# Kernel tuning notes

Measured on AMD Instinct MI355X. Metric: run time of the kernel, lower is better.

The kernel has to match this reference:

```python
import jax, jax.numpy as jnp
import numpy as np
import math

D_MODEL = 1024
NUM_HEADS = 16
NUM_LAYERS = 4
D_FF = 4096
TEXT_DIM = 512
B, SV, ST = 4, 2048, 100
EPS = 1e-5


def positional_encoding(seq_len, d):
    pos = jnp.arange(seq_len, dtype=jnp.float32)[:, None]
    div = jnp.exp(jnp.arange(0, d, 2, dtype=jnp.float32) * (-math.log(10000.0) / d))
    pe = jnp.zeros((seq_len, d), dtype=jnp.float32)
    pe = pe.at[:, 0::2].set(jnp.sin(pos * div))
    pe = pe.at[:, 1::2].set(jnp.cos(pos * div))
    return pe  # [seq_len, d]


def layer_norm(x, g, b):
    mu = jnp.mean(x, axis=-1, keepdims=True)
    var = jnp.mean(jnp.square(x - mu), axis=-1, keepdims=True)
    return (x - mu) * jax.lax.rsqrt(var + EPS) * g + b


def setup_inputs() -> dict:
    key = jax.random.key(0)
    ks = jax.random.split(key, 24)
    s = 0.02
    inp = {
        "video": jax.random.normal(ks[0], (B, SV, D_MODEL), jnp.float32),
        "text": jax.random.normal(ks[1], (B, ST, TEXT_DIM), jnp.float32),
        "text_mask": jnp.ones((B, ST), jnp.int32),
        # stacked per-layer params, weights stored [in, out]
        "Wq_w": jax.random.normal(ks[2], (NUM_LAYERS, D_MODEL, D_MODEL)) * s,
        "Wq_b": jnp.zeros((NUM_LAYERS, D_MODEL)),
        "Wk_w": jax.random.normal(ks[3], (NUM_LAYERS, TEXT_DIM, D_MODEL)) * s,
        "Wk_b": jnp.zeros((NUM_LAYERS, D_MODEL)),
        "Wv_w": jax.random.normal(ks[4], (NUM_LAYERS, TEXT_DIM, D_MODEL)) * s,
        "Wv_b": jnp.zeros((NUM_LAYERS, D_MODEL)),
        "Wo_w": jax.random.normal(ks[5], (NUM_LAYERS, D_MODEL, D_MODEL)) * s,
        "Wo_b": jnp.zeros((NUM_LAYERS, D_MODEL)),
        "fc1_w": jax.random.normal(ks[6], (NUM_LAYERS, D_MODEL, D_FF)) * s,
        "fc1_b": jnp.zeros((NUM_LAYERS, D_FF)),
        "fc2_w": jax.random.normal(ks[7], (NUM_LAYERS, D_FF, D_MODEL)) * s,
        "fc2_b": jnp.zeros((NUM_LAYERS, D_MODEL)),
        "n2_g": jnp.ones((NUM_LAYERS, D_MODEL)),
        "n2_b": jnp.zeros((NUM_LAYERS, D_MODEL)),
        "n3_g": jnp.ones((NUM_LAYERS, D_MODEL)),
        "n3_b": jnp.zeros((NUM_LAYERS, D_MODEL)),
    }
    return inp


def cross_attn_layer(video, text, mask, wq, bq, wk, bk, wv, bv, wo, bo):
    Bv, Sq, D = video.shape
    H, dk = NUM_HEADS, D_MODEL // NUM_HEADS
    q = (video @ wq + bq).reshape(Bv, Sq, H, dk).transpose(0, 2, 1, 3)  # bhqd
    k = (text @ wk + bk).reshape(Bv, -1, H, dk).transpose(0, 2, 1, 3)   # bhkd
    v = (text @ wv + bv).reshape(Bv, -1, H, dk).transpose(0, 2, 1, 3)
    scores = jnp.einsum("bhqd,bhkd->bhqk", q, k) / math.sqrt(dk)
    scores = jnp.where(mask, scores, jnp.float32(-1e9))
    probs = jax.nn.softmax(scores, axis=-1)
    out = jnp.einsum("bhqk,bhkd->bhqd", probs, v)
    out = out.transpose(0, 2, 1, 3).reshape(Bv, Sq, D)
    return out @ wo + bo


def reference(video, text, text_mask, Wq_w, Wq_b, Wk_w, Wk_b, Wv_w, Wv_b,
              Wo_w, Wo_b, fc1_w, fc1_b, fc2_w, fc2_b, n2_g, n2_b, n3_g, n3_b):
    video = video + positional_encoding(SV, D_MODEL)[None, :video.shape[1]]
    text = text + positional_encoding(ST, TEXT_DIM)[None, :text.shape[1]]
    mask = (text_mask != 0)[:, None, None, :]  # [B,1,1,St]
    for l in range(NUM_LAYERS):
        attn = cross_attn_layer(video, text, mask,
                                Wq_w[l], Wq_b[l], Wk_w[l], Wk_b[l],
                                Wv_w[l], Wv_b[l], Wo_w[l], Wo_b[l])
        video = layer_norm(video + attn, n2_g[l], n2_b[l])
        ff = jax.nn.relu(video @ fc1_w[l] + fc1_b[l]) @ fc2_w[l] + fc2_b[l]
        video = layer_norm(video + ff, n3_g[l], n3_b[l])
    return video
```

## Files before the change

### kernel.cpp

```cpp
#include <hip/hip_runtime.h>
#include <cstdint>
#include <cstddef>

typedef unsigned short u16;
typedef __attribute__((ext_vector_type(8))) __bf16 bf16x8;
typedef __attribute__((ext_vector_type(4))) float f32x4;

__device__ __forceinline__ f32x4 mfma_16x16x32(bf16x8 a, bf16x8 b, f32x4 c) {
  return __builtin_amdgcn_mfma_f32_16x16x32_bf16(a, b, c, 0, 0, 0);
}

__device__ __forceinline__ u16 f2bf(float f) {
  union { float f; uint32_t u; } c; c.f = f;
  uint32_t u = c.u + 0x7FFFu + ((c.u >> 16) & 1u);
  return (u16)(u >> 16);
}

__device__ __forceinline__ float bf2f(u16 x) {
  union { uint32_t u; float f; } c; c.u = ((uint32_t)x) << 16;
  return c.f;
}

__device__ __forceinline__ void gload_lds16(const void* g, void* l) {
  __builtin_amdgcn_global_load_lds(
      (__attribute__((address_space(1))) void*)(uintptr_t)g,
      (__attribute__((address_space(3))) void*)l, 16, 0, 0);
}

template<bool OUT_BF16, bool RELU, bool ACC>
__global__ __launch_bounds__(512, 2) void gemm8p(
    const u16* __restrict__ A, int lda, const u16* __restrict__ Bt, int ldb,
    const float* __restrict__ bias, void* Cout, int ldc,
    int M, int N, int K)
{
  constexpr int BM = 256, BN = 128, BK = 64;
  constexpr int TILE = (BM + BN) * BK;
  __shared__ u16 lds[3 * TILE];

  const int tid = threadIdx.x;
  const int lane = tid & 63, wave = tid >> 6;
  const int wm = wave >> 1, wn = wave & 1;
  const int m0 = blockIdx.x * BM, n0 = blockIdx.y * BN;

  const u16* gA[4];
  const u16* gB[2];
  #pragma unroll
  for (int i = 0; i < 4; i++) {
    int c = tid + i * 512, r = c >> 3, q = c & 7;
    gA[i] = A + (size_t)(m0 + r) * lda + ((q ^ (r & 7)) * 8);
  }
  #pragma unroll
  for (int i = 0; i < 2; i++) {
    int c = tid + i * 512, r = c >> 3, q = c & 7;
    gB[i] = Bt + (size_t)(n0 + r) * ldb + ((q ^ (r & 7)) * 8);
  }

  const int NT = K >> 6;

  auto STAGE = [&](int t, int buf, int piece) {
    u16* Sb = &lds[buf * TILE];
    const int ko = t * 64;
    if (piece == 0) {
      gload_lds16(gA[0] + ko, Sb + tid * 8);
      gload_lds16(gA[1] + ko, Sb + (tid + 512) * 8);
    } else if (piece == 1) {
      gload_lds16(gA[2] + ko, Sb + (tid + 1024) * 8);
      gload_lds16(gA[3] + ko, Sb + (tid + 1536) * 8);
    } else {
      gload_lds16(gB[0] + ko, Sb + BM * 64 + tid * 8);
      gload_lds16(gB[1] + ko, Sb + BM * 64 + (tid + 512) * 8);
    }
  };

  const int fr = lane & 15, g = lane >> 4;
  const int sx = fr & 7;

  f32x4 acc[4][4];
  #pragma unroll
  for (int m = 0; m < 4; m++)
    #pragma unroll
    for (int n = 0; n < 4; n++) acc[m][n] = f32x4{0.f, 0.f, 0.f, 0.f};

  STAGE(0, 0, 0); STAGE(0, 0, 1); STAGE(0, 0, 2);
  STAGE(1, 1, 0); STAGE(1, 1, 1); STAGE(1, 1, 2);
  asm volatile("s_waitcnt vmcnt(6)" ::: "memory");
  __builtin_amdgcn_s_barrier();
  __builtin_amdgcn_sched_barrier(0);

  int cur = 0;
  for (int t = 0; t < NT; ++t) {
    const u16* As = &lds[cur * TILE];
    const u16* Bs = As + BM * 64;
    const bool st = (t + 2 < NT);
    int sbuf = cur + 2; if (sbuf >= 3) sbuf -= 3;

    bf16x8 bf[4], afA[2], afB[2];
    const int arow0 = wm * 64 + fr;
    const int brow0 = wn * 64 + fr;

    #pragma unroll
    for (int nf = 0; nf < 4; nf++)
      bf[nf] = *(const bf16x8*)(Bs + (brow0 + nf * 16) * 64 + ((g ^ sx) * 8));
    #pragma unroll
    for (int mf = 0; mf < 2; mf++)
      afA[mf] = *(const bf16x8*)(As + (arow0 + mf * 16) * 64 + ((g ^ sx) * 8));
    if (st) STAGE(t + 2, sbuf, 0);
    __builtin_amdgcn_s_barrier();
    asm volatile("s_waitcnt lgkmcnt(0)" ::: "memory");
    __builtin_amdgcn_sched_barrier(0);
    __builtin_amdgcn_s_setprio(1);
    #pragma unroll
    for (int mf = 0; mf < 2; mf++)
      #pragma unroll
      for (int nf = 0; nf < 4; nf++)
        acc[mf][nf] = mfma_16x16x32(afA[mf], bf[nf], acc[mf][nf]);
    __builtin_amdgcn_s_setprio(0);
    __builtin_amdgcn_s_barrier();

    #pragma unroll
    for (int mf = 0; mf < 2; mf++)
      afB[mf] = *(const bf16x8*)(As + (arow0 + (mf + 2) * 16) * 64 + ((g ^ sx) * 8));
    if (st) STAGE(t + 2, sbuf, 1);
    __builtin_amdgcn_s_barrier();
    asm volatile("s_waitcnt lgkmcnt(0)" ::: "memory");
    __builtin_amdgcn_sched_barrier(0);
    __builtin_amdgcn_s_setprio(1);
    #pragma unroll
    for (int mf = 0; mf < 2; mf++)
      #pragma unroll
      for (int nf = 0; nf < 4; nf++)
        acc[mf + 2][nf] = mfma_16x16x32(afB[mf], bf[nf], acc[mf + 2][nf]);
    __builtin_amdgcn_s_setprio(0);
    __builtin_amdgcn_s_barrier();

    #pragma unroll
    for (int nf = 0; nf < 4; nf++)
      bf[nf] = *(const bf16x8*)(Bs + (brow0 + nf * 16) * 64 + (((4 + g) ^ sx) * 8));
    #pragma unroll
    for (int mf = 0; mf < 2; mf++)
      afA[mf] = *(const bf16x8*)(As + (arow0 + mf * 16) * 64 + (((4 + g) ^ sx) * 8));
    if (st) STAGE(t + 2, sbuf, 2);
    __builtin_amdgcn_s_barrier();
    asm volatile("s_waitcnt lgkmcnt(0)" ::: "memory");
    __builtin_amdgcn_sched_barrier(0);
    __builtin_amdgcn_s_setprio(1);
    #pragma unroll
    for (int mf = 0; mf < 2; mf++)
      #pragma unroll
      for (int nf = 0; nf < 4; nf++)
        acc[mf][nf] = mfma_16x16x32(afA[mf], bf[nf], acc[mf][nf]);
    __builtin_amdgcn_s_setprio(0);
    __builtin_amdgcn_s_barrier();

    #pragma unroll
    for (int mf = 0; mf < 2; mf++)
      afB[mf] = *(const bf16x8*)(As + (arow0 + (mf + 2) * 16) * 64 + (((4 + g) ^ sx) * 8));
    __builtin_amdgcn_s_barrier();
    asm volatile("s_waitcnt lgkmcnt(0)" ::: "memory");
    __builtin_amdgcn_sched_barrier(0);
    __builtin_amdgcn_s_setprio(1);
    #pragma unroll
    for (int mf = 0; mf < 2; mf++)
      #pragma unroll
      for (int nf = 0; nf < 4; nf++)
        acc[mf + 2][nf] = mfma_16x16x32(afB[mf], bf[nf], acc[mf + 2][nf]);
    __builtin_amdgcn_s_setprio(0);
    if (st) asm volatile("s_waitcnt vmcnt(6)" ::: "memory");
    else    asm volatile("s_waitcnt vmcnt(0)" ::: "memory");
    __builtin_amdgcn_sched_barrier(0);
    __builtin_amdgcn_s_barrier();
    __builtin_amdgcn_sched_barrier(0);

    cur = cur + 1 == 3 ? 0 : cur + 1;
  }

  #pragma unroll
  for (int nf = 0; nf < 4; nf++) {
    const int gcol = n0 + wn * 64 + nf * 16 + fr;
    const float bv = bias ? bias[gcol] : 0.f;
    #pragma unroll
    for (int mf = 0; mf < 4; mf++) {
      #pragma unroll
      for (int r = 0; r < 4; r++) {
        const int grow = m0 + wm * 64 + mf * 16 + g * 4 + r;
        float v = acc[mf][nf][r] + bv;
        if (ACC) v += bf2f(((const u16*)Cout)[(size_t)grow * ldc + gcol]);
        if (RELU) v = fmaxf(v, 0.f);
        if (OUT_BF16) ((u16*)Cout)[(size_t)grow * ldc + gcol] = f2bf(v);
        else         ((float*)Cout)[(size_t)grow * ldc + gcol] = v;
      }
    }
  }
}

template<bool TRANS>
__global__ __launch_bounds__(256, 2) void gemm_bt(
    const u16* __restrict__ A, int lda, const u16* __restrict__ Bt, int ldb,
    const float* __restrict__ bias, u16* Cout, int ldc,
    int M, int N, int K)
{
  __shared__ u16 ldsA[128 * 32];
  __shared__ u16 ldsB[128 * 32];

  const int tid = threadIdx.x;
  const int lane = tid & 63, wave = tid >> 6;
  const int wr = wave >> 1, wc = wave & 1;
  const int m0 = blockIdx.x * 128, n0 = blockIdx.y * 128;

  const int c0 = tid, c1 = tid + 256;
  const int ar0 = c0 >> 2, ak0 = (c0 & 3) * 8;
  const int ar1 = c1 >> 2, ak1 = (c1 & 3) * 8;

  const bool av0 = (m0 + ar0) < M;
  const bool av1 = (m0 + ar1) < M;
  const u16* Ag0 = A + (size_t)(m0 + ar0) * lda + ak0;
  const u16* Ag1 = A + (size_t)(m0 + ar1) * lda + ak1;
  const u16* Bg0 = Bt + (size_t)(n0 + ar0) * ldb + ak0;
  const u16* Bg1 = Bt + (size_t)(n0 + ar1) * ldb + ak1;

  f32x4 acc[4][4] = {};
  const int fr = lane & 15, fo = (lane >> 4) * 8;

  for (int k0 = 0; k0 < K; k0 += 32) {
    if (av0) gload_lds16(Ag0 + k0, &ldsA[c0 * 8]);
    if (av1) gload_lds16(Ag1 + k0, &ldsA[c1 * 8]);
    gload_lds16(Bg0 + k0, &ldsB[c0 * 8]);
    gload_lds16(Bg1 + k0, &ldsB[c1 * 8]);
    asm volatile("s_waitcnt vmcnt(0)" ::: "memory");
    __syncthreads();

    bf16x8 af[4], bfr[4];
    #pragma unroll
    for (int m = 0; m < 4; m++)
      af[m] = *(const bf16x8*)&ldsA[(wr * 64 + m * 16 + fr) * 32 + fo];
    #pragma unroll
    for (int n = 0; n < 4; n++)
      bfr[n] = *(const bf16x8*)&ldsB[(wc * 64 + n * 16 + fr) * 32 + fo];
    #pragma unroll
    for (int m = 0; m < 4; m++)
      #pragma unroll
      for (int n = 0; n < 4; n++)
        acc[m][n] = mfma_16x16x32(af[m], bfr[n], acc[m][n]);
    __syncthreads();
  }

  const int g = lane >> 4;
  #pragma unroll
  for (int m = 0; m < 4; m++) {
    #pragma unroll
    for (int n = 0; n < 4; n++) {
      const int gcol = n0 + wc * 64 + n * 16 + fr;
      const float bv = bias[gcol];
      #pragma unroll
      for (int r = 0; r < 4; r++) {
        const int grow = m0 + wr * 64 + m * 16 + g * 4 + r;
        if (grow < M) {
          float v = acc[m][n][r] + bv;
          if (TRANS) {
            int bb = grow / 100, jj = grow - bb * 100;
            int h = gcol >> 6, d = gcol & 63;
            Cout[(size_t)(((bb * 16 + h) * 64 + d)) * 128 + jj] = f2bf(v);
          } else {
            Cout[(size_t)grow * ldc + gcol] = f2bf(v);
          }
        }
      }
    }
  }
}

__global__ void wconv_t(const float* __restrict__ src, u16* __restrict__ dst,
                        int K, int N)
{
  __shared__ float tile[32][33];
  const int n0 = blockIdx.x * 32, k0 = blockIdx.y * 32;
  const int tx = threadIdx.x, ty = threadIdx.y;
  #pragma unroll
  for (int i = 0; i < 4; i++)
    tile[ty + i * 8][tx] = src[(size_t)(k0 + ty + i * 8) * N + n0 + tx];
  __syncthreads();
  #pragma unroll
  for (int i = 0; i < 4; i++)
    dst[(size_t)(n0 + ty + i * 8) * K + k0 + tx] = f2bf(tile[tx][ty + i * 8]);
}

__global__ __launch_bounds__(256) void pe_video_k(const float* __restrict__ video,
                                                  u16* __restrict__ vbf)
{
  const int r = blockIdx.x;
  const int s = r & 2047;
  const int d0 = threadIdx.x * 4;
  const size_t base = (size_t)r * 1024 + d0;
  float4 v = *(const float4*)&video[base];
  const float coef = -9.210340371976184f / 1024.f;
  float o[4];
  float in[4] = {v.x, v.y, v.z, v.w};
  #pragma unroll
  for (int i = 0; i < 4; i++) {
    int d = d0 + i;
    int j = d >> 1;
    float dv = expf((float)(2 * j) * coef);
    float arg = (float)s * dv;
    float pe = (d & 1) ? cosf(arg) : sinf(arg);
    o[i] = in[i] + pe;
  }
  uint2 pk;
  pk.x = (uint32_t)f2bf(o[0]) | ((uint32_t)f2bf(o[1]) << 16);
  pk.y = (uint32_t)f2bf(o[2]) | ((uint32_t)f2bf(o[3]) << 16);
  *(uint2*)&vbf[base] = pk;
}

__global__ __launch_bounds__(128) void pe_text_k(const float* __restrict__ text,
                                                 u16* __restrict__ tbf)
{
  const int r = blockIdx.x;
  const int s = r % 100;
  const int d0 = threadIdx.x * 4;
  const size_t base = (size_t)r * 512 + d0;
  float4 v = *(const float4*)&text[base];
  const float coef = -9.210340371976184f / 512.f;
  float o[4];
  float in[4] = {v.x, v.y, v.z, v.w};
  #pragma unroll
  for (int i = 0; i < 4; i++) {
    int d = d0 + i;
    int j = d >> 1;
    float dv = expf((float)(2 * j) * coef);
    float arg = (float)s * dv;
    float pe = (d & 1) ? cosf(arg) : sinf(arg);
    o[i] = in[i] + pe;
  }
  uint2 pk;
  pk.x = (uint32_t)f2bf(o[0]) | ((uint32_t)f2bf(o[1]) << 16);
  pk.y = (uint32_t)f2bf(o[2]) | ((uint32_t)f2bf(o[3]) << 16);
  *(uint2*)&tbf[base] = pk;
}

template<bool LAST>
__global__ __launch_bounds__(256) void ln2(const u16* __restrict__ xin,
                                           const u16* __restrict__ delta,
                                           const float* __restrict__ gamma,
                                           const float* __restrict__ beta,
                                           u16* __restrict__ xbf,
                                           float* __restrict__ fout)
{
  const int row = blockIdx.x;
  const size_t base = (size_t)row * 1024;
  const int t = threadIdx.x;
  const int d0 = t * 4;
  uint2 xv = *(const uint2*)&xin[base + d0];
  uint2 dv = *(const uint2*)&delta[base + d0];
  float v0 = bf2f((u16)(xv.x & 0xFFFF)) + bf2f((u16)(dv.x & 0xFFFF));
  float v1 = bf2f((u16)(xv.x >> 16))    + bf2f((u16)(dv.x >> 16));
  float v2 = bf2f((u16)(xv.y & 0xFFFF)) + bf2f((u16)(dv.y & 0xFFFF));
  float v3 = bf2f((u16)(xv.y >> 16))    + bf2f((u16)(dv.y >> 16));
  float s = v0 + v1 + v2 + v3;
  float q = v0 * v0 + v1 * v1 + v2 * v2 + v3 * v3;
  #pragma unroll
  for (int d = 32; d >= 1; d >>= 1) { s += __shfl_xor(s, d); q += __shfl_xor(q, d); }
  __shared__ float red[8];
  const int lane = t & 63, w = t >> 6;
  if (lane == 0) { red[w] = s; red[4 + w] = q; }
  __syncthreads();
  float S = red[0] + red[1] + red[2] + red[3];
  float Qs = red[4] + red[5] + red[6] + red[7];
  const float mu = S * (1.f / 1024.f);
  const float var = Qs * (1.f / 1024.f) - mu * mu;
  const float rs = rsqrtf(var + 1e-5f);
  float4 gv = *(const float4*)&gamma[d0];
  float4 bv = *(const float4*)&beta[d0];
  float o0 = (v0 - mu) * rs * gv.x + bv.x;
  float o1 = (v1 - mu) * rs * gv.y + bv.y;
  float o2 = (v2 - mu) * rs * gv.z + bv.z;
  float o3 = (v3 - mu) * rs * gv.w + bv.w;
  if (LAST) {
    *(float4*)&fout[base + d0] = make_float4(o0, o1, o2, o3);
  } else {
    uint2 pk;
    pk.x = (uint32_t)f2bf(o0) | ((uint32_t)f2bf(o1) << 16);
    pk.y = (uint32_t)f2bf(o2) | ((uint32_t)f2bf(o3) << 16);
    *(uint2*)&xbf[base + d0] = pk;
  }
}

__global__ __launch_bounds__(256) void attn_v2(
    const u16* __restrict__ Q, const u16* __restrict__ Kb,
    const u16* __restrict__ Vtb, const int* __restrict__ mask,
    u16* __restrict__ Out)
{
  __shared__ u16 ldsP[64 * 136];

  const int tid = threadIdx.x, lane = tid & 63, w = tid >> 6;
  const int qb = blockIdx.x, bh = blockIdx.y;
  const int b = bh >> 4, h = bh & 15;
  const int fr = lane & 15, g = lane >> 4, fo = g * 8;

  const size_t qrow = (size_t)(b * 2048 + qb * 64 + w * 16 + fr) * 1024 + h * 64;
  bf16x8 qf0 = *(const bf16x8*)&Q[qrow + fo];
  bf16x8 qf1 = *(const bf16x8*)&Q[qrow + 32 + fo];

  float madd[7];
  #pragma unroll
  for (int t = 0; t < 7; t++) {
    int col = t * 16 + fr;
    int mv = (col < 100) ? mask[b * 100 + col] : 0;
    madd[t] = mv ? 0.f : -1e30f;
  }

  float sc[7][4];
  #pragma unroll
  for (int t = 0; t < 7; t++) {
    int col = t * 16 + fr;
    int jr = (col < 100) ? col : 99;
    const u16* kp = Kb + (size_t)(b * 100 + jr) * 1024 + h * 64;
    bf16x8 kf0 = *(const bf16x8*)&kp[fo];
    bf16x8 kf1 = *(const bf16x8*)&kp[32 + fo];
    f32x4 a = {};
    a = mfma_16x16x32(qf0, kf0, a);
    a = mfma_16x16x32(qf1, kf1, a);
    #pragma unroll
    for (int r = 0; r < 4; r++)
      sc[t][r] = a[r] * 0.125f + madd[t];
  }

  #pragma unroll
  for (int r = 0; r < 4; r++) {
    float m = sc[0][r];
    #pragma unroll
    for (int t = 1; t < 7; t++) m = fmaxf(m, sc[t][r]);
    #pragma unroll
    for (int d = 8; d >= 1; d >>= 1) m = fmaxf(m, __shfl_xor(m, d));
    float ssum = 0.f;
    #pragma unroll
    for (int t = 0; t < 7; t++) { float p = __expf(sc[t][r] - m); sc[t][r] = p; ssum += p; }
    #pragma unroll
    for (int d = 8; d >= 1; d >>= 1) ssum += __shfl_xor(ssum, d);
    float is = 1.f / ssum;
    #pragma unroll
    for (int t = 0; t < 7; t++)
      ldsP[(w * 16 + g * 4 + r) * 136 + t * 16 + fr] = f2bf(sc[t][r] * is);
  }
  {
    u16* zp = &ldsP[(w * 16 + fr) * 136 + 112 + g * 6];
    #pragma unroll
    for (int i = 0; i < 6; i++) zp[i] = 0;
  }

  bf16x8 pa[4];
  #pragma unroll
  for (int kk = 0; kk < 4; kk++)
    pa[kk] = *(const bf16x8*)&ldsP[(w * 16 + fr) * 136 + kk * 32 + fo];
  const u16* vtbase = Vtb + (size_t)bh * 64 * 128;
  #pragma unroll
  for (int nt = 0; nt < 4; nt++) {
    f32x4 a = {};
    #pragma unroll
    for (int kk = 0; kk < 4; kk++) {
      bf16x8 vf = *(const bf16x8*)&vtbase[(size_t)(nt * 16 + fr) * 128 + kk * 32 + fo];
      a = mfma_16x16x32(pa[kk], vf, a);
    }
    #pragma unroll
    for (int r = 0; r < 4; r++) {
      size_t orow = (size_t)(b * 2048 + qb * 64 + w * 16 + g * 4 + r) * 1024 + h * 64 + nt * 16 + fr;
      Out[orow] = f2bf(a[r]);
    }
  }
}

extern "C" void kernel_launch(void* const* d_in, const int* in_sizes, int n_in,
                              void* d_out, int out_size, void* d_ws, size_t ws_size,
                              hipStream_t stream) {
  const float* video = (const float*)d_in[0];
  const float* text  = (const float*)d_in[1];
  const int*   text_mask = (const int*)d_in[2];
  const float* Wq_w = (const float*)d_in[3];
  const float* Wq_b = (const float*)d_in[4];
  const float* Wk_w = (const float*)d_in[5];
  const float* Wk_b = (const float*)d_in[6];
  const float* Wv_w = (const float*)d_in[7];
  const float* Wv_b = (const float*)d_in[8];
  const float* Wo_w = (const float*)d_in[9];
  const float* Wo_b = (const float*)d_in[10];
  const float* fc1_w = (const float*)d_in[11];
  const float* fc1_b = (const float*)d_in[12];
  const float* fc2_w = (const float*)d_in[13];
  const float* fc2_b = (const float*)d_in[14];
  const float* n2_g = (const float*)d_in[15];
  const float* n2_b = (const float*)d_in[16];
  const float* n3_g = (const float*)d_in[17];
  const float* n3_b = (const float*)d_in[18];

  char* ws = (char*)d_ws;
  size_t off = 0;
  auto alloc = [&](size_t bytes) {
    char* p = ws + off;
    off += (bytes + 255) & ~(size_t)255;
    return p;
  };
  u16* vbf = (u16*)alloc((size_t)8192 * 1024 * 2);
  u16* tbf = (u16*)alloc((size_t)400 * 512 * 2);
  u16* wqT = (u16*)alloc((size_t)1024 * 1024 * 2);
  u16* wkT = (u16*)alloc((size_t)1024 * 512 * 2);
  u16* wvT = (u16*)alloc((size_t)1024 * 512 * 2);
  u16* woT = (u16*)alloc((size_t)1024 * 1024 * 2);
  u16* f1T = (u16*)alloc((size_t)4096 * 1024 * 2);
  u16* f2T = (u16*)alloc((size_t)1024 * 4096 * 2);
  char* S = alloc((size_t)35192832);
  u16* qbf  = (u16*)S;
  u16* kbf  = (u16*)(S + 16777216);
  u16* abf  = (u16*)(S + 16777216 + 1638400);
  u16* h1c  = (u16*)S;
  u16* vtb  = (u16*)alloc((size_t)64 * 64 * 128 * 2);
  u16* dbf  = (u16*)alloc((size_t)8192 * 1024 * 2);
  float* fout = (float*)d_out;

  hipMemsetAsync(vtb, 0, (size_t)64 * 64 * 128 * 2, stream);

  pe_video_k<<<8192, 256, 0, stream>>>(video, vbf);
  pe_text_k<<<400, 128, 0, stream>>>(text, tbf);

  dim3 tb(32, 8, 1);
  for (int l = 0; l < 4; ++l) {
    wconv_t<<<dim3(32, 32), tb, 0, stream>>>(Wq_w + (size_t)l * 1024 * 1024, wqT, 1024, 1024);
    wconv_t<<<dim3(32, 16), tb, 0, stream>>>(Wk_w + (size_t)l * 512 * 1024, wkT, 512, 1024);
    wconv_t<<<dim3(32, 16), tb, 0, stream>>>(Wv_w + (size_t)l * 512 * 1024, wvT, 512, 1024);
    wconv_t<<<dim3(32, 32), tb, 0, stream>>>(Wo_w + (size_t)l * 1024 * 1024, woT, 1024, 1024);
    wconv_t<<<dim3(128, 32), tb, 0, stream>>>(fc1_w + (size_t)l * 1024 * 4096, f1T, 1024, 4096);
    wconv_t<<<dim3(32, 128), tb, 0, stream>>>(fc2_w + (size_t)l * 4096 * 1024, f2T, 4096, 1024);

    gemm8p<true, false, false><<<dim3(32, 8), 512, 0, stream>>>(
        vbf, 1024, wqT, 1024, Wq_b + l * 1024, qbf, 1024, 8192, 1024, 1024);
    gemm_bt<false><<<dim3(4, 8), 256, 0, stream>>>(
        tbf, 512, wkT, 512, Wk_b + l * 1024, kbf, 1024, 400, 1024, 512);
    gemm_bt<true><<<dim3(4, 8), 256, 0, stream>>>(
        tbf, 512, wvT, 512, Wv_b + l * 1024, vtb, 1024, 400, 1024, 512);
    attn_v2<<<dim3(32, 64), 256, 0, stream>>>(qbf, kbf, vtb, text_mask, abf);
    gemm8p<true, false, false><<<dim3(32, 8), 512, 0, stream>>>(
        abf, 1024, woT, 1024, Wo_b + l * 1024, dbf, 1024, 8192, 1024, 1024);
    ln2<false><<<8192, 256, 0, stream>>>(vbf, dbf, n2_g + l * 1024, n2_b + l * 1024, vbf, nullptr);

    for (int c = 0; c < 2; ++c) {
      gemm8p<true, true, false><<<dim3(32, 16), 512, 0, stream>>>(
          vbf, 1024, f1T + (size_t)c * 2048 * 1024, 1024,
          fc1_b + l * 4096 + c * 2048, h1c, 2048, 8192, 2048, 1024);
      if (c == 0)
        gemm8p<true, false, false><<<dim3(32, 8), 512, 0, stream>>>(
            h1c, 2048, f2T + (size_t)c * 2048, 4096,
            fc2_b + l * 1024, dbf, 1024, 8192, 1024, 2048);
      else
        gemm8p<true, false, true><<<dim3(32, 8), 512, 0, stream>>>(
            h1c, 2048, f2T + (size_t)c * 2048, 4096,
            nullptr, dbf, 1024, 8192, 1024, 2048);
    }
    if (l == 3)
      ln2<true><<<8192, 256, 0, stream>>>(vbf, dbf, n3_g + l * 1024, n3_b + l * 1024, nullptr, fout);
    else
      ln2<false><<<8192, 256, 0, stream>>>(vbf, dbf, n3_g + l * 1024, n3_b + l * 1024, vbf, nullptr);
  }
}
```

Baseline: 1.336 ms.

## Add 256x256-tile double-buffered GEMM kernel and use it for fc1

```diff
diff --git a/kernel.cpp b/kernel.cpp
--- a/kernel.cpp
+++ b/kernel.cpp
@@ -25,6 +25,170 @@
   __builtin_amdgcn_global_load_lds(
       (__attribute__((address_space(1))) void*)(uintptr_t)g,
       (__attribute__((address_space(3))) void*)l, 16, 0, 0);
+}
+
+template<bool OUT_BF16, bool RELU>
+__global__ __launch_bounds__(512, 2) void gemm256(
+    const u16* __restrict__ A, int lda, const u16* __restrict__ Bt, int ldb,
+    const float* __restrict__ bias, void* Cout, int ldc,
+    int M, int N, int K)
+{
+  constexpr int BM = 256, BK = 64;
+  constexpr int TILE = 512 * BK;
+  __shared__ u16 lds[2 * TILE];
+
+  const int tid = threadIdx.x;
+  const int lane = tid & 63, wave = tid >> 6;
+  const int wm = wave >> 2, wn = wave & 3;
+  const int m0 = blockIdx.x * 256, n0 = blockIdx.y * 256;
+
+  const u16* gA[4];
+  const u16* gB[4];
+  #pragma unroll
+  for (int i = 0; i < 4; i++) {
+    int c = tid + i * 512, r = c >> 3, q = c & 7;
+    gA[i] = A + (size_t)(m0 + r) * lda + ((q ^ (r & 7)) * 8);
+    gB[i] = Bt + (size_t)(n0 + r) * ldb + ((q ^ (r & 7)) * 8);
+  }
+
+  const int NT = K >> 6;
+
+  auto STAGE_P0 = [&](int t, int buf) {
+    u16* Sb = &lds[buf * TILE];
+    const int ko = t * 64;
+    gload_lds16(gA[0] + ko, Sb + (tid) * 8);
+    gload_lds16(gA[2] + ko, Sb + (tid + 1024) * 8);
+    gload_lds16(gB[0] + ko, Sb + BM * 64 + (tid) * 8);
+    gload_lds16(gB[1] + ko, Sb + BM * 64 + (tid + 512) * 8);
+  };
+  auto STAGE_P1 = [&](int t, int buf) {
+    u16* Sb = &lds[buf * TILE];
+    const int ko = t * 64;
+    gload_lds16(gB[2] + ko, Sb + BM * 64 + (tid + 1024) * 8);
+    gload_lds16(gB[3] + ko, Sb + BM * 64 + (tid + 1536) * 8);
+    gload_lds16(gA[1] + ko, Sb + (tid + 512) * 8);
+    gload_lds16(gA[3] + ko, Sb + (tid + 1536) * 8);
+  };
+
+  const int fr = lane & 15, g = lane >> 4;
+  const int sx = fr & 7;
+
+  f32x4 acc[8][4];
+  #pragma unroll
+  for (int m = 0; m < 8; m++)
+    #pragma unroll
+    for (int n = 0; n < 4; n++) acc[m][n] = f32x4{0.f, 0.f, 0.f, 0.f};
+
+  STAGE_P0(0, 0);
+  STAGE_P1(0, 0);
+  asm volatile("s_waitcnt vmcnt(2)" ::: "memory");
+  __builtin_amdgcn_s_barrier();
+  __builtin_amdgcn_sched_barrier(0);
+
+  int cur = 0;
+  for (int t = 0; t < NT; ++t) {
+    const u16* As = &lds[cur * TILE];
+    const u16* Bs = As + BM * 64;
+    const bool stg = (t + 1 < NT);
+    const int nxt = cur ^ 1;
+
+    const int arow0 = wm * 128 + fr;
+    const int brow0 = wn * 64 + fr;
+    bf16x8 bf[4], af[4];
+
+    #pragma unroll
+    for (int nf = 0; nf < 4; nf++)
+      bf[nf] = *(const bf16x8*)(Bs + (brow0 + nf * 16) * 64 + ((g ^ sx) * 8));
+    #pragma unroll
+    for (int mf = 0; mf < 4; mf++)
+      af[mf] = *(const bf16x8*)(As + (arow0 + mf * 16) * 64 + ((g ^ sx) * 8));
+    if (stg) STAGE_P0(t + 1, nxt);
+    __builtin_amdgcn_s_barrier();
+    asm volatile("s_waitcnt lgkmcnt(0)" ::: "memory");
+    __builtin_amdgcn_sched_barrier(0);
+    __builtin_amdgcn_s_setprio(1);
+    #pragma unroll
+    for (int mf = 0; mf < 4; mf++)
+      #pragma unroll
+      for (int nf = 0; nf < 4; nf++)
+        acc[mf][nf] = mfma_16x16x32(af[mf], bf[nf], acc[mf][nf]);
+    __builtin_amdgcn_s_setprio(0);
+    if (stg) asm volatile("s_waitcnt vmcnt(4)" ::: "memory");
+    else     asm volatile("s_waitcnt vmcnt(0)" ::: "memory");
+    __builtin_amdgcn_sched_barrier(0);
+    __builtin_amdgcn_s_barrier();
+
+    #pragma unroll
+    for (int mf = 0; mf < 4; mf++)
+      af[mf] = *(const bf16x8*)(As + (arow0 + (mf + 4) * 16) * 64 + ((g ^ sx) * 8));
+    if (stg) STAGE_P1(t + 1, nxt);
+    __builtin_amdgcn_s_barrier();
+    asm volatile("s_waitcnt lgkmcnt(0)" ::: "memory");
+    __builtin_amdgcn_sched_barrier(0);
+    __builtin_amdgcn_s_setprio(1);
+    #pragma unroll
+    for (int mf = 0; mf < 4; mf++)
+      #pragma unroll
+      for (int nf = 0; nf < 4; nf++)
+        acc[mf + 4][nf] = mfma_16x16x32(af[mf], bf[nf], acc[mf + 4][nf]);
+    __builtin_amdgcn_s_setprio(0);
+    __builtin_amdgcn_s_barrier();
+
+    #pragma unroll
+    for (int nf = 0; nf < 4; nf++)
+      bf[nf] = *(const bf16x8*)(Bs + (brow0 + nf * 16) * 64 + (((4 + g) ^ sx) * 8));
+    #pragma unroll
+    for (int mf = 0; mf < 4; mf++)
+      af[mf] = *(const bf16x8*)(As + (arow0 + mf * 16) * 64 + (((4 + g) ^ sx) * 8));
+    __builtin_amdgcn_s_barrier();
+    asm volatile("s_waitcnt lgkmcnt(0)" ::: "memory");
+    __builtin_amdgcn_sched_barrier(0);
+    __builtin_amdgcn_s_setprio(1);
+    #pragma unroll
+    for (int mf = 0; mf < 4; mf++)
+      #pragma unroll
+      for (int nf = 0; nf < 4; nf++)
+        acc[mf][nf] = mfma_16x16x32(af[mf], bf[nf], acc[mf][nf]);
+    __builtin_amdgcn_s_setprio(0);
+    __builtin_amdgcn_s_barrier();
+
+    #pragma unroll
+    for (int mf = 0; mf < 4; mf++)
+      af[mf] = *(const bf16x8*)(As + (arow0 + (mf + 4) * 16) * 64 + (((4 + g) ^ sx) * 8));
+    __builtin_amdgcn_s_barrier();
+    asm volatile("s_waitcnt lgkmcnt(0)" ::: "memory");
+    __builtin_amdgcn_sched_barrier(0);
+    __builtin_amdgcn_s_setprio(1);
+    #pragma unroll
+    for (int mf = 0; mf < 4; mf++)
+      #pragma unroll
+      for (int nf = 0; nf < 4; nf++)
+        acc[mf + 4][nf] = mfma_16x16x32(af[mf], bf[nf], acc[mf + 4][nf]);
+    __builtin_amdgcn_s_setprio(0);
+    if (stg) asm volatile("s_waitcnt vmcnt(2)" ::: "memory");
+    __builtin_amdgcn_sched_barrier(0);
+    __builtin_amdgcn_s_barrier();
+    __builtin_amdgcn_sched_barrier(0);
+
+    cur = nxt;
+  }
+
+  #pragma unroll
+  for (int nf = 0; nf < 4; nf++) {
+    const int gcol = n0 + wn * 64 + nf * 16 + fr;
+    const float bv = bias ? bias[gcol] : 0.f;
+    #pragma unroll
+    for (int mf = 0; mf < 8; mf++) {
+      #pragma unroll
+      for (int r = 0; r < 4; r++) {
+        const int grow = m0 + wm * 128 + mf * 16 + g * 4 + r;
+        float v = acc[mf][nf][r] + bv;
+        if (RELU) v = fmaxf(v, 0.f);
+        if (OUT_BF16) ((u16*)Cout)[(size_t)grow * ldc + gcol] = f2bf(v);
+        else         ((float*)Cout)[(size_t)grow * ldc + gcol] = v;
+      }
+    }
+  }
 }
 
 template<bool OUT_BF16, bool RELU, bool ACC>
@@ -540,7 +704,7 @@
     ln2<false><<<8192, 256, 0, stream>>>(vbf, dbf, n2_g + l * 1024, n2_b + l * 1024, vbf, nullptr);
 
     for (int c = 0; c < 2; ++c) {
-      gemm8p<true, true, false><<<dim3(32, 16), 512, 0, stream>>>(
+      gemm256<true, true><<<dim3(32, 8), 512, 0, stream>>>(
           vbf, 1024, f1T + (size_t)c * 2048 * 1024, 1024,
           fc1_b + l * 4096 + c * 2048, h1c, 2048, 8192, 2048, 1024);
       if (c == 0)
```

After: 1.331 ms. No clear change (-0.4%).
